# Kernel optimization log

Hardware: AMD Instinct MI355X
Metric: run time of the kernel (lower is better)

The kernel has to match this reference:

```python
import jax, jax.numpy as jnp
import numpy as np
import math

B, N, DIM, H, DH = 4, 1024, 512, 8, 64
INNER = H * DH
TEMP = 0.1
REG_LAMBDA = 0.3
LARGE_NEG = -1.0e9


def setup_inputs() -> dict:
    key = jax.random.key(0)
    ks = jax.random.split(key, 10)
    x = jax.random.normal(ks[0], (B, N, DIM), dtype=jnp.float32)
    # binary channel mask with guaranteed self-connection on the diagonal
    m = jax.random.randint(ks[1], (B, N, N), 0, 2, dtype=jnp.int32)
    eye_i = jnp.eye(N, dtype=jnp.int32)[None]
    attn_mask = jnp.maximum(m, eye_i)
    s = 0.02
    Wq = jax.random.normal(ks[2], (DIM, INNER), dtype=jnp.float32) * s
    bq = jnp.zeros((INNER,), dtype=jnp.float32)
    Wk = jax.random.normal(ks[3], (DIM, INNER), dtype=jnp.float32) * s
    bk = jnp.zeros((INNER,), dtype=jnp.float32)
    Wv = jax.random.normal(ks[4], (DIM, INNER), dtype=jnp.float32) * s
    bv = jnp.zeros((INNER,), dtype=jnp.float32)
    Wo = jax.random.normal(ks[5], (INNER, DIM), dtype=jnpp_dummy()) * s if False else jax.random.normal(ks[5], (INNER, DIM), dtype=jnp.float32) * s
    bo = jnp.zeros((DIM,), dtype=jnp.float32)
    return {"x": x, "attn_mask": attn_mask, "Wq": Wq, "bq": bq, "Wk": Wk,
            "bk": bk, "Wv": Wv, "bv": bv, "Wo": Wo, "bo": bo}


def jnp_dummy():
    return jnp.float32


def _split_heads(t):
    # [b, n, h*d] -> [b, h, n, d]
    return t.reshape(t.shape[0], t.shape[1], H, DH).transpose(0, 2, 1, 3)


def _dynamical_contrastive_loss(scores, attn_mask_f, norm_matrix):
    # cosine similarity matrix (scores / |q||k|)
    cos = scores / norm_matrix
    e = jnp.exp(cos / TEMP)                                   # [b,h,n,n]
    pos = (e * attn_mask_f[:, None]).sum(-1)                  # [b,h,n]
    allsum = e.sum(-1)                                        # [b,h,n]
    clustering = -jnp.log(pos / allsum)
    eye = jnp.eye(N, dtype=attn_mask_f.dtype)
    regular = jnp.abs(attn_mask_f - eye[None]).sum((-2, -1)) / (N * (N - 1))
    return clustering.mean() + REG_LAMBDA * regular.mean()


def reference(x, attn_mask, Wq, bq, Wk, bk, Wv, bv, Wo, bo):
    q = _split_heads(x @ Wq + bq)  # [b,h,n,d]
    k = _split_heads(x @ Wk + bk)
    v = _split_heads(x @ Wv + bv)
    scale = 1.0 / math.sqrt(DH)

    scores = jnp.einsum('bhid,bhjd->bhij', q, k)
    q_norm = jnp.linalg.norm(q, axis=-1, keepdims=True)       # [b,h,n,1]
    k_norm = jnp.linalg.norm(k, axis=-1, keepdims=True)
    norm_matrix = q_norm * jnp.swapaxes(k_norm, -1, -2)       # [b,h,n,n]

    am = attn_mask.astype(scores.dtype)[:, None]              # [b,1,n,n]
    masked_scores = scores * am + (1.0 - am) * LARGE_NEG
    # faithful replication of the all-blocked-row special case
    # (-1e9 is finite so this is a no-op unless scores contain -inf)
    row_all_blocked = jnp.all(jnp.isneginf(masked_scores), axis=-1, keepdims=True)
    masked_scores = jnp.where(row_all_blocked, jnp.zeros_like(masked_scores), masked_scores)

    dcl = _dynamical_contrastive_loss(scores, attn_mask.astype(scores.dtype), norm_matrix)

    attn = jax.nn.softmax(masked_scores * scale, axis=-1)
    out = jnp.einsum('bhij,bhjd->bhid', attn, v)
    out = out.transpose(0, 2, 1, 3).reshape(x.shape[0], x.shape[1], INNER)
    # dropout is identity in eval mode
    return out @ Wo + bo, attn, dcl
```

## Files before the change

kernel.cpp:

```cpp
#include <hip/hip_runtime.h>
#include <hip/hip_bf16.h>
#include <math.h>

#define BB 4
#define NTOK 1024
#define DIMD 512
#define HH 8
#define DH 64
#define INNER 512
#define BH (BB*HH)
#define ROWS (BB*NTOK)
#define SCALE 0.125f
#define INV_TEMP 10.0f

typedef __bf16 bf16_t;
using bf16x4 = __attribute__((ext_vector_type(4))) __bf16;
using bf16x8 = __attribute__((ext_vector_type(8))) __bf16;
using f32x4  = __attribute__((ext_vector_type(4))) float;

__device__ __forceinline__ int swz(int row, int e) { return e ^ ((row & 7) << 3); }

__device__ __forceinline__ void gload_lds16(const bf16_t* g, bf16_t* l)
{
    __builtin_amdgcn_global_load_lds(
        (const __attribute__((address_space(1))) void*)g,
        (__attribute__((address_space(3))) void*)l, 16, 0, 0);
}

template<int TM, int TN, int MT, int NT>
__device__ __forceinline__ void gemm_core(
    const bf16_t* __restrict__ A, int ldA,
    const bf16_t* __restrict__ B, int ldB, int K,
    bf16_t* As, bf16_t* Bs, f32x4 (&acc)[MT][NT])
{
    const int t = threadIdx.x;
    const int w = t >> 6, l = t & 63;
    constexpr int WGN = TN / (NT * 16);
    const int wm = w / WGN, wn = w % WGN;
    const int lrow = l & 15, lk = (l >> 4) * 8;
    constexpr int ASZ = TM * 32, BSZ = TN * 32;

    auto stage = [&](int k0, int buf) {
        #pragma unroll
        for (int it = 0; it < TM / 64; ++it)
            gload_lds16(&A[(size_t)((t >> 2) + it * 64) * ldA + k0 + (t & 3) * 8],
                        As + buf * ASZ + ((size_t)it * 256 + w * 64) * 8);
        #pragma unroll
        for (int it = 0; it < TN / 64; ++it)
            gload_lds16(&B[(size_t)((t >> 2) + it * 64) * ldB + k0 + (t & 3) * 8],
                        Bs + buf * BSZ + ((size_t)it * 256 + w * 64) * 8);
    };

    stage(0, 0);
    __syncthreads();
    for (int k0 = 0; k0 < K; k0 += 32) {
        const int cur = (k0 >> 5) & 1;
        if (k0 + 32 < K) stage(k0 + 32, cur ^ 1);
        const bf16_t* Ac = As + cur * ASZ;
        const bf16_t* Bc = Bs + cur * BSZ;
        bf16x8 af[MT], bf[NT];
        #pragma unroll
        for (int mt = 0; mt < MT; ++mt)
            af[mt] = *(const bf16x8*)&Ac[(wm * MT * 16 + mt * 16 + lrow) * 32 + lk];
        #pragma unroll
        for (int nt = 0; nt < NT; ++nt)
            bf[nt] = *(const bf16x8*)&Bc[(wn * NT * 16 + nt * 16 + lrow) * 32 + lk];
        #pragma unroll
        for (int mt = 0; mt < MT; ++mt)
            #pragma unroll
            for (int nt = 0; nt < NT; ++nt)
                acc[mt][nt] = __builtin_amdgcn_mfma_f32_16x16x32_bf16(
                    af[mt], bf[nt], acc[mt][nt], 0, 0, 0);
        __syncthreads();
    }
}

__global__ __launch_bounds__(256) void prep_kernel(
    const float* __restrict__ x,
    const float* __restrict__ Wq, const float* __restrict__ Wk,
    const float* __restrict__ Wv, const float* __restrict__ Wo,
    const int* __restrict__ mask,
    bf16_t* __restrict__ xb, bf16_t* __restrict__ wt,
    unsigned int* __restrict__ mp)
{
    __shared__ float tile[32][33];
    const int bid = blockIdx.x, t = threadIdx.x;
    if (bid < 2048) {
        int idx = bid * 256 + t;
        float4 v = ((const float4*)x)[idx];
        bf16x4 o = { (bf16_t)v.x, (bf16_t)v.y, (bf16_t)v.z, (bf16_t)v.w };
        ((bf16x4*)xb)[idx] = o;
    } else if (bid < 3072) {
        int f = bid - 2048;
        int bx = f & 15, by = (f >> 4) & 15, z = f >> 8;
        const float* src = (z == 0) ? Wq : (z == 1) ? Wk : (z == 2) ? Wv : Wo;
        bf16_t* dst = wt + (size_t)z * DIMD * INNER;
        const int tx = t & 31, ty = t >> 5;
        const int rBase = by * 32, cBase = bx * 32;
        #pragma unroll
        for (int i = 0; i < 4; ++i)
            tile[ty + i * 8][tx] = src[(size_t)(rBase + ty + i * 8) * INNER + cBase + tx];
        __syncthreads();
        #pragma unroll
        for (int i = 0; i < 4; ++i)
            dst[(size_t)(cBase + ty + i * 8) * DIMD + rBase + tx] = (bf16_t)tile[tx][ty + i * 8];
    } else {
        int f = bid - 3072;
        int rr = f & 255, b = f >> 8;
        const int* mb = mask + ((size_t)(b * NTOK + rr * 4)) * NTOK;
        #pragma unroll
        for (int u = 0; u < 4; ++u) {
            int col = u * 256 + t;
            unsigned int o = (unsigned)mb[col]
                           | ((unsigned)mb[NTOK + col] << 8)
                           | ((unsigned)mb[2 * NTOK + col] << 16)
                           | ((unsigned)mb[3 * NTOK + col] << 24);
            mp[((size_t)b * 256 + rr) * NTOK + col] = o;
        }
    }
}

__global__ __launch_bounds__(256) void qkv_gemm(
    const bf16_t* __restrict__ xb, const bf16_t* __restrict__ wt,
    const float* __restrict__ bq, const float* __restrict__ bk,
    const float* __restrict__ bv,
    bf16_t* __restrict__ qb, bf16_t* __restrict__ kb, bf16_t* __restrict__ vt,
    float* __restrict__ iqn, float* __restrict__ ikn)
{
    __shared__ __align__(16) bf16_t As[2 * 64 * 32];
    __shared__ __align__(16) bf16_t Bs[2 * 128 * 32];
    const int z = blockIdx.z;
    const bf16_t* Bp = wt + (size_t)z * DIMD * INNER;
    const float* bias = (z == 0) ? bq : (z == 1) ? bk : bv;
    const int rowBase = blockIdx.y * 64, colBase = blockIdx.x * 128;

    f32x4 acc[2][4] = {};
    gemm_core<64, 128, 2, 4>(xb + (size_t)rowBase * DIMD, DIMD,
                             Bp + (size_t)colBase * DIMD, DIMD, DIMD,
                             As, Bs, acc);

    const int l = threadIdx.x & 63, w = threadIdx.x >> 6;
    const int wm = w >> 1, wn = w & 1;
    float nsum[2][4] = {};
    #pragma unroll
    for (int mt = 0; mt < 2; ++mt)
        #pragma unroll
        for (int nt = 0; nt < 4; ++nt)
            #pragma unroll
            for (int r = 0; r < 4; ++r) {
                int grow = rowBase + wm * 32 + mt * 16 + (l >> 4) * 4 + r;
                int gcol = colBase + wn * 64 + nt * 16 + (l & 15);
                float val = acc[mt][nt][r] + bias[gcol];
                bf16_t vb16 = (bf16_t)val;
                int b = grow >> 10, n = grow & 1023, h = gcol >> 6, d = gcol & 63;
                if (z == 0)
                    qb[(((size_t)b * HH + h) * NTOK + n) * DH + d] = vb16;
                else if (z == 1)
                    kb[(((size_t)b * HH + h) * NTOK + n) * DH + d] = vb16;
                else
                    vt[(((size_t)b * HH + h) * DH + d) * NTOK + n] = vb16;
                if (z < 2) { float vb = (float)vb16; nsum[mt][r] += vb * vb; }
            }
    if (z < 2) {
        float* dst = (z == 0) ? iqn : ikn;
        const int h = (colBase >> 6) + wn;
        #pragma unroll
        for (int mt = 0; mt < 2; ++mt)
            #pragma unroll
            for (int r = 0; r < 4; ++r) {
                float s = nsum[mt][r];
                s += __shfl_xor(s, 8); s += __shfl_xor(s, 4);
                s += __shfl_xor(s, 2); s += __shfl_xor(s, 1);
                if ((l & 15) == 0) {
                    int grow = rowBase + wm * 32 + mt * 16 + (l >> 4) * 4 + r;
                    int b = grow >> 10, n = grow & 1023;
                    dst[((size_t)b * HH + h) * NTOK + n] = 1.0f / sqrtf(s);
                }
            }
    }
}

__global__ __launch_bounds__(512) void attn_fused(
    const bf16_t* __restrict__ qb, const bf16_t* __restrict__ kb,
    const bf16_t* __restrict__ vt, const unsigned int* __restrict__ mp,
    const float* __restrict__ iqn, const float* __restrict__ ikn,
    float* __restrict__ attnf, bf16_t* __restrict__ ctxb,
    float* __restrict__ cl, float* __restrict__ rg)
{
    __shared__ __align__(16) bf16_t Ks[2][64 * 64];
    __shared__ __align__(16) bf16_t Vs[2][64 * 64];
    __shared__ __align__(16) bf16_t Ps[8][16 * 64];
    __shared__ float4 sred[8][16];
    const int bh = blockIdx.y;
    const int b = bh >> 3, h = bh & 7;
    const int rowBase = blockIdx.x * 64;
    const bf16_t* Q = qb + (size_t)bh * NTOK * DH;
    const bf16_t* K = kb + (size_t)bh * NTOK * DH;
    const bf16_t* V = vt + (size_t)bh * DH * NTOK;
    const float* iknr = ikn + (size_t)bh * NTOK;
    const int t = threadIdx.x, w = t >> 6, l = t & 63;
    const int half = w >> 2, rw = w & 3;
    const int l15 = l & 15, q = l >> 4;
    bf16_t* Pw = Ps[w];

    bf16x8 af[2];
    {
        const bf16_t* qrow = Q + (size_t)(rowBase + rw * 16 + l15) * DH + q * 8;
        af[0] = *(const bf16x8*)(qrow);
        af[1] = *(const bf16x8*)(qrow + 32);
    }
    const int tok = rowBase + rw * 16 + q * 4;
    float iqn4[4];
    #pragma unroll
    for (int r = 0; r < 4; ++r)
        iqn4[r] = iqn[(size_t)bh * NTOK + tok + r];
    const unsigned int* mrow = mp + ((size_t)b * 256 + (tok >> 2)) * NTOK;

    float alls[4] = {}, pos[4] = {}, esum[4] = {}, regf[4] = {};

    for (int tt = 0; tt < 8; ++tt) {
        const int col0 = half * 512 + tt * 64;
        #pragma unroll
        for (int u = 0; u < 2; ++u) {
            int g = (u * 8 + w) * 64 + l;
            int hh = g >> 9, kr = (g >> 3) & 63, ci = g & 7;
            gload_lds16(K + (size_t)(hh * 512 + tt * 64 + kr) * DH + ((ci * 8) ^ ((kr & 7) << 3)),
                        &Ks[0][0] + (size_t)(u * 8 + w) * 512);
        }
        unsigned int mm4[4]; float ik4[4];
        #pragma unroll
        for (int nt = 0; nt < 4; ++nt) {
            int c = col0 + nt * 16 + l15;
            mm4[nt] = mrow[c];
            ik4[nt] = iknr[c];
        }
        __syncthreads();
        f32x4 sacc[4] = {};
        #pragma unroll
        for (int ks = 0; ks < 2; ++ks) {
            int koff = ks * 32 + q * 8;
            #pragma unroll
            for (int nt = 0; nt < 4; ++nt) {
                int kr = nt * 16 + l15;
                bf16x8 bfk = *(const bf16x8*)&Ks[half][kr * 64 + swz(kr, koff)];
                sacc[nt] = __builtin_amdgcn_mfma_f32_16x16x32_bf16(af[ks], bfk, sacc[nt], 0, 0, 0);
            }
        }
        #pragma unroll
        for (int nt = 0; nt < 4; ++nt) {
            float ik = ik4[nt];
            unsigned int mm = mm4[nt];
            #pragma unroll
            for (int r = 0; r < 4; ++r) {
                float s = sacc[nt][r];
                float mbit = (float)((mm >> (8 * r)) & 1u);
                float e1 = __expf(s * iqn4[r] * ik * INV_TEMP);
                float e2 = __expf(s * SCALE);
                alls[r] += e1;
                pos[r]  += e1 * mbit;
                esum[r] += e2 * mbit;
                regf[r] += mbit;
            }
        }
        __syncthreads();
    }
    #pragma unroll
    for (int r = 0; r < 4; ++r) {
        #pragma unroll
        for (int off = 8; off; off >>= 1) {
            alls[r] += __shfl_xor(alls[r], off);
            pos[r]  += __shfl_xor(pos[r], off);
            esum[r] += __shfl_xor(esum[r], off);
            regf[r] += __shfl_xor(regf[r], off);
        }
    }
    if (l15 == 0) {
        #pragma unroll
        for (int r = 0; r < 4; ++r)
            sred[w][q * 4 + r] = make_float4(alls[r], pos[r], esum[r], regf[r]);
    }
    __syncthreads();
    float inv4[4];
    #pragma unroll
    for (int r = 0; r < 4; ++r) {
        float4 o = sred[w ^ 4][q * 4 + r];
        float allsT = alls[r] + o.x;
        float posT  = pos[r]  + o.y;
        float esumT = esum[r] + o.z;
        float regT  = regf[r] + o.w;
        inv4[r] = 1.0f / esumT;
        if (half == 0 && l15 == 0) {
            int rowG = bh * NTOK + tok + r;
            cl[rowG] = logf(allsT) - logf(posT);
            if (h == 0) rg[b * NTOK + tok + r] = regT - 1.0f;
        }
    }

    float* prow = attnf + ((size_t)bh * NTOK + tok) * NTOK;
    f32x4 cacc[4] = {};
    for (int tt = 0; tt < 8; ++tt) {
        const int col0 = half * 512 + tt * 64;
        #pragma unroll
        for (int u = 0; u < 2; ++u) {
            int g = (u * 8 + w) * 64 + l;
            int hh = g >> 9, kr = (g >> 3) & 63, ci = g & 7;
            gload_lds16(K + (size_t)(hh * 512 + tt * 64 + kr) * DH + ((ci * 8) ^ ((kr & 7) << 3)),
                        &Ks[0][0] + (size_t)(u * 8 + w) * 512);
        }
        #pragma unroll
        for (int u = 0; u < 2; ++u) {
            int g = (u * 8 + w) * 64 + l;
            int hh = g >> 9, d = (g >> 3) & 63, ci = g & 7;
            gload_lds16(V + (size_t)d * NTOK + hh * 512 + tt * 64 + ((ci * 8) ^ ((d & 7) << 3)),
                        &Vs[0][0] + (size_t)(u * 8 + w) * 512);
        }
        unsigned int mm4[4];
        #pragma unroll
        for (int nt = 0; nt < 4; ++nt)
            mm4[nt] = mrow[col0 + nt * 16 + l15];
        __syncthreads();
        f32x4 sacc[4] = {};
        #pragma unroll
        for (int ks = 0; ks < 2; ++ks) {
            int koff = ks * 32 + q * 8;
            #pragma unroll
            for (int nt = 0; nt < 4; ++nt) {
                int kr = nt * 16 + l15;
                bf16x8 bfk = *(const bf16x8*)&Ks[half][kr * 64 + swz(kr, koff)];
                sacc[nt] = __builtin_amdgcn_mfma_f32_16x16x32_bf16(af[ks], bfk, sacc[nt], 0, 0, 0);
            }
        }
        #pragma unroll
        for (int nt = 0; nt < 4; ++nt) {
            int c = nt * 16 + l15;
            unsigned int mm = mm4[nt];
            #pragma unroll
            for (int r = 0; r < 4; ++r) {
                float p = ((mm >> (8 * r)) & 1u)
                        ? __expf(sacc[nt][r] * SCALE) * inv4[r] : 0.0f;
                prow[(size_t)r * NTOK + col0 + c] = p;
                int pr = q * 4 + r;
                Pw[pr * 64 + swz(pr, c)] = (bf16_t)p;
            }
        }
        #pragma unroll
        for (int ks = 0; ks < 2; ++ks) {
            int koff = ks * 32 + q * 8;
            bf16x8 afp = *(const bf16x8*)&Pw[l15 * 64 + swz(l15, koff)];
            #pragma unroll
            for (int nt = 0; nt < 4; ++nt) {
                int d = nt * 16 + l15;
                bf16x8 bfv = *(const bf16x8*)&Vs[half][d * 64 + swz(d, koff)];
                cacc[nt] = __builtin_amdgcn_mfma_f32_16x16x32_bf16(afp, bfv, cacc[nt], 0, 0, 0);
            }
        }
        __syncthreads();
    }
    float* cred = (float*)&Ps[0][0];
    if (half == 1) {
        #pragma unroll
        for (int nt = 0; nt < 4; ++nt)
            #pragma unroll
            for (int r = 0; r < 4; ++r)
                cred[(size_t)rw * 1024 + (q * 4 + r) * 64 + nt * 16 + l15] = cacc[nt][r];
    }
    __syncthreads();
    if (half == 0) {
        #pragma unroll
        for (int nt = 0; nt < 4; ++nt)
            #pragma unroll
            for (int r = 0; r < 4; ++r) {
                float v = cacc[nt][r] + cred[(size_t)rw * 1024 + (q * 4 + r) * 64 + nt * 16 + l15];
                int n = tok + r;
                int d = nt * 16 + l15;
                ctxb[((size_t)b * NTOK + n) * INNER + h * DH + d] = (bf16_t)v;
            }
    }
}

__device__ __forceinline__ float block_sum(float v, float* sh)
{
    #pragma unroll
    for (int off = 32; off; off >>= 1) v += __shfl_down(v, off);
    __syncthreads();
    if ((threadIdx.x & 63) == 0) sh[threadIdx.x >> 6] = v;
    __syncthreads();
    return sh[0] + sh[1] + sh[2] + sh[3];
}

__global__ __launch_bounds__(256) void out_gemm(
    const bf16_t* __restrict__ ctxb, const bf16_t* __restrict__ wt,
    const float* __restrict__ bo, float* __restrict__ outp,
    const float* __restrict__ cl, const float* __restrict__ rg,
    float* __restrict__ dcl)
{
    __shared__ __align__(16) bf16_t As[2 * 64 * 32];
    __shared__ __align__(16) bf16_t Bs[2 * 128 * 32];
    __shared__ float sh4[4];
    const int rowBase = blockIdx.y * 64, colBase = blockIdx.x * 128;
    const bf16_t* Wot = wt + (size_t)3 * DIMD * INNER;

    f32x4 acc[2][4] = {};
    gemm_core<64, 128, 2, 4>(ctxb + (size_t)rowBase * INNER, INNER,
                             Wot + (size_t)colBase * INNER, INNER, INNER,
                             As, Bs, acc);

    const int l = threadIdx.x & 63, w = threadIdx.x >> 6;
    const int wm = w >> 1, wn = w & 1;
    #pragma unroll
    for (int mt = 0; mt < 2; ++mt)
        #pragma unroll
        for (int nt = 0; nt < 4; ++nt)
            #pragma unroll
            for (int r = 0; r < 4; ++r) {
                int grow = rowBase + wm * 32 + mt * 16 + (l >> 4) * 4 + r;
                int gcol = colBase + wn * 64 + nt * 16 + (l & 15);
                outp[(size_t)grow * DIMD + gcol] = acc[mt][nt][r] + bo[gcol];
            }

    if (blockIdx.x == 0 && blockIdx.y == 0) {
        float s1 = 0.f, s2 = 0.f;
        for (int idx = threadIdx.x; idx < BH * NTOK; idx += 256) s1 += cl[idx];
        for (int idx = threadIdx.x; idx < BB * NTOK; idx += 256) s2 += rg[idx];
        __syncthreads();
        s1 = block_sum(s1, sh4);
        s2 = block_sum(s2, sh4);
        if (threadIdx.x == 0) {
            dcl[0] = s1 * (1.0f / (float)(BB * HH * NTOK))
                   + 0.3f * s2 * (1.0f / ((float)NTOK * (float)(NTOK - 1) * (float)BB));
        }
    }
}

extern "C" void kernel_launch(void* const* d_in, const int* in_sizes, int n_in,
                              void* d_out, int out_size, void* d_ws, size_t ws_size,
                              hipStream_t stream)
{
    const float* x  = (const float*)d_in[0];
    const int* mask = (const int*)d_in[1];
    const float* Wq = (const float*)d_in[2];
    const float* bq = (const float*)d_in[3];
    const float* Wk = (const float*)d_in[4];
    const float* bk = (const float*)d_in[5];
    const float* Wv = (const float*)d_in[6];
    const float* bv = (const float*)d_in[7];
    const float* Wo = (const float*)d_in[8];
    const float* bo = (const float*)d_in[9];

    float* out   = (float*)d_out;
    float* attnf = out + (size_t)ROWS * DIMD;
    float* dcl   = attnf + (size_t)BH * NTOK * NTOK;

    char* wsb = (char*)d_ws;
    bf16_t* xb    = (bf16_t*)wsb;
    bf16_t* wt    = xb + (size_t)ROWS * DIMD;
    bf16_t* qb    = wt + (size_t)4 * DIMD * INNER;
    bf16_t* kb    = qb + (size_t)BH * NTOK * DH;
    bf16_t* vt    = kb + (size_t)BH * NTOK * DH;
    bf16_t* ctxb  = vt + (size_t)BH * NTOK * DH;
    float*  iqn   = (float*)(ctxb + (size_t)ROWS * INNER);
    float*  ikn   = iqn + BH * NTOK;
    float*  cl    = ikn + BH * NTOK;
    float*  rg    = cl + BH * NTOK;
    unsigned int* mpk = (unsigned int*)(rg + BB * NTOK);

    dim3 blk(256);
    prep_kernel<<<dim3(4096), blk, 0, stream>>>(x, Wq, Wk, Wv, Wo, mask, xb, wt, mpk);
    qkv_gemm<<<dim3(4, 64, 3), blk, 0, stream>>>(xb, wt, bq, bk, bv, qb, kb, vt, iqn, ikn);
    attn_fused<<<dim3(16, 32), dim3(512), 0, stream>>>(qb, kb, vt, mpk, iqn, ikn, attnf, ctxb, cl, rg);
    out_gemm<<<dim3(4, 64), blk, 0, stream>>>(ctxb, wt, bo, out, cl, rg, dcl);
}
```

Baseline: 271.1 us.

## Double-buffer K tiles in attention loops and remap blocks across XCDs

```diff
diff --git a/kernel.cpp b/kernel.cpp
--- a/kernel.cpp
+++ b/kernel.cpp
@@ -187,13 +187,17 @@
     float* __restrict__ attnf, bf16_t* __restrict__ ctxb,
     float* __restrict__ cl, float* __restrict__ rg)
 {
-    __shared__ __align__(16) bf16_t Ks[2][64 * 64];
+    __shared__ __align__(16) bf16_t Kbuf[2][2][64 * 64];
     __shared__ __align__(16) bf16_t Vs[2][64 * 64];
     __shared__ __align__(16) bf16_t Ps[8][16 * 64];
     __shared__ float4 sred[8][16];
-    const int bh = blockIdx.y;
+
+    const int wg = blockIdx.x;
+    const int sz = (wg & 7) * 64 + (wg >> 3);
+    const int bh = sz >> 4;
+    const int rowBase = (sz & 15) * 64;
+
     const int b = bh >> 3, h = bh & 7;
-    const int rowBase = blockIdx.x * 64;
     const bf16_t* Q = qb + (size_t)bh * NTOK * DH;
     const bf16_t* K = kb + (size_t)bh * NTOK * DH;
     const bf16_t* V = vt + (size_t)bh * DH * NTOK;
@@ -203,6 +207,25 @@
     const int l15 = l & 15, q = l >> 4;
     bf16_t* Pw = Ps[w];
 
+    auto stageK = [&](int tt, int buf) {
+        #pragma unroll
+        for (int u = 0; u < 2; ++u) {
+            int g = (u * 8 + w) * 64 + l;
+            int hh = g >> 9, kr = (g >> 3) & 63, ci = g & 7;
+            gload_lds16(K + (size_t)(hh * 512 + tt * 64 + kr) * DH + ((ci * 8) ^ ((kr & 7) << 3)),
+                        &Kbuf[buf][0][0] + (size_t)(u * 8 + w) * 512);
+        }
+    };
+    auto stageV = [&](int tt) {
+        #pragma unroll
+        for (int u = 0; u < 2; ++u) {
+            int g = (u * 8 + w) * 64 + l;
+            int hh = g >> 9, d = (g >> 3) & 63, ci = g & 7;
+            gload_lds16(V + (size_t)d * NTOK + hh * 512 + tt * 64 + ((ci * 8) ^ ((d & 7) << 3)),
+                        &Vs[0][0] + (size_t)(u * 8 + w) * 512);
+        }
+    };
+
     bf16x8 af[2];
     {
         const bf16_t* qrow = Q + (size_t)(rowBase + rw * 16 + l15) * DH + q * 8;
@@ -218,15 +241,11 @@
 
     float alls[4] = {}, pos[4] = {}, esum[4] = {}, regf[4] = {};
 
+    stageK(0, 0);
+    __syncthreads();
     for (int tt = 0; tt < 8; ++tt) {
         const int col0 = half * 512 + tt * 64;
-        #pragma unroll
-        for (int u = 0; u < 2; ++u) {
-            int g = (u * 8 + w) * 64 + l;
-            int hh = g >> 9, kr = (g >> 3) & 63, ci = g & 7;
-            gload_lds16(K + (size_t)(hh * 512 + tt * 64 + kr) * DH + ((ci * 8) ^ ((kr & 7) << 3)),
-                        &Ks[0][0] + (size_t)(u * 8 + w) * 512);
-        }
+        if (tt < 7) stageK(tt + 1, (tt + 1) & 1);
         unsigned int mm4[4]; float ik4[4];
         #pragma unroll
         for (int nt = 0; nt < 4; ++nt) {
@@ -234,7 +253,7 @@
             mm4[nt] = mrow[c];
             ik4[nt] = iknr[c];
         }
-        __syncthreads();
+        const bf16_t* Kh = &Kbuf[tt & 1][half][0];
         f32x4 sacc[4] = {};
         #pragma unroll
         for (int ks = 0; ks < 2; ++ks) {
@@ -242,7 +261,7 @@
             #pragma unroll
             for (int nt = 0; nt < 4; ++nt) {
                 int kr = nt * 16 + l15;
-                bf16x8 bfk = *(const bf16x8*)&Ks[half][kr * 64 + swz(kr, koff)];
+                bf16x8 bfk = *(const bf16x8*)&Kh[kr * 64 + swz(kr, koff)];
                 sacc[nt] = __builtin_amdgcn_mfma_f32_16x16x32_bf16(af[ks], bfk, sacc[nt], 0, 0, 0);
             }
         }
@@ -298,27 +317,17 @@
 
     float* prow = attnf + ((size_t)bh * NTOK + tok) * NTOK;
     f32x4 cacc[4] = {};
+    stageK(0, 0);
+    __syncthreads();
     for (int tt = 0; tt < 8; ++tt) {
         const int col0 = half * 512 + tt * 64;
-        #pragma unroll
-        for (int u = 0; u < 2; ++u) {
-            int g = (u * 8 + w) * 64 + l;
-            int hh = g >> 9, kr = (g >> 3) & 63, ci = g & 7;
-            gload_lds16(K + (size_t)(hh * 512 + tt * 64 + kr) * DH + ((ci * 8) ^ ((kr & 7) << 3)),
-                        &Ks[0][0] + (size_t)(u * 8 + w) * 512);
-        }
-        #pragma unroll
-        for (int u = 0; u < 2; ++u) {
-            int g = (u * 8 + w) * 64 + l;
-            int hh = g >> 9, d = (g >> 3) & 63, ci = g & 7;
-            gload_lds16(V + (size_t)d * NTOK + hh * 512 + tt * 64 + ((ci * 8) ^ ((d & 7) << 3)),
-                        &Vs[0][0] + (size_t)(u * 8 + w) * 512);
-        }
+        stageV(tt);
+        if (tt < 7) stageK(tt + 1, (tt + 1) & 1);
         unsigned int mm4[4];
         #pragma unroll
         for (int nt = 0; nt < 4; ++nt)
             mm4[nt] = mrow[col0 + nt * 16 + l15];
-        __syncthreads();
+        const bf16_t* Kh = &Kbuf[tt & 1][half][0];
         f32x4 sacc[4] = {};
         #pragma unroll
         for (int ks = 0; ks < 2; ++ks) {
@@ -326,7 +335,7 @@
             #pragma unroll
             for (int nt = 0; nt < 4; ++nt) {
                 int kr = nt * 16 + l15;
-                bf16x8 bfk = *(const bf16x8*)&Ks[half][kr * 64 + swz(kr, koff)];
+                bf16x8 bfk = *(const bf16x8*)&Kh[kr * 64 + swz(kr, koff)];
                 sacc[nt] = __builtin_amdgcn_mfma_f32_16x16x32_bf16(af[ks], bfk, sacc[nt], 0, 0, 0);
             }
         }
@@ -343,6 +352,7 @@
                 Pw[pr * 64 + swz(pr, c)] = (bf16_t)p;
             }
         }
+        __syncthreads();
         #pragma unroll
         for (int ks = 0; ks < 2; ++ks) {
             int koff = ks * 32 + q * 8;
@@ -467,6 +477,6 @@
     dim3 blk(256);
     prep_kernel<<<dim3(4096), blk, 0, stream>>>(x, Wq, Wk, Wv, Wo, mask, xb, wt, mpk);
     qkv_gemm<<<dim3(4, 64, 3), blk, 0, stream>>>(xb, wt, bq, bk, bv, qb, kb, vt, iqn, ikn);
-    attn_fused<<<dim3(16, 32), dim3(512), 0, stream>>>(qb, kb, vt, mpk, iqn, ikn, attnf, ctxb, cl, rg);
+    attn_fused<<<dim3(512), dim3(512), 0, stream>>>(qb, kb, vt, mpk, iqn, ikn, attnf, ctxb, cl, rg);
     out_gemm<<<dim3(4, 64), blk, 0, stream>>>(ctxb, wt, bo, out, cl, rg, dcl);
 }
```

Measured after the change: 279.1 us. 1.03x slower.
